# Kernel tuning notes

Hardware: AMD Instinct MI355X
Metric: run time of the kernel (lower is better)

## Reference

```python
import jax, jax.numpy as jnp
import numpy as np

B, S, T, D, H, FF = 2, 512, 64, 256, 8, 1024
DK = D // H
EPS = 1e-5


def setup_inputs() -> dict:
    key = jax.random.key(0)
    ks = jax.random.split(key, 24)
    sc = 1.0 / np.sqrt(D)
    inp = {"x": jax.random.normal(ks[0], (B, S, T, D), jnp.float32)}
    names = ["tq", "tk", "tv", "to", "sq", "sk", "sv", "so"]
    for i, n in enumerate(names):
        inp[n + "_w"] = jax.random.normal(ks[1 + 2 * i], (D, D), jnp.float32) * sc
        inp[n + "_b"] = jax.random.normal(ks[2 + 2 * i], (D,), jnp.float32) * sc
    inp["fc1_w"] = jax.random.normal(ks[17], (D, FF), jnp.float32) * sc
    inp["fc1_b"] = jnp.zeros((FF,), jnp.float32)
    inp["fc2_w"] = jax.random.normal(ks[18], (FF, D), jnp.float32) * (1.0 / np.sqrt(FF))
    inp["fc2_b"] = jnp.zeros((D,), jnp.float32)
    inp["ln1_w"] = jnp.ones((D,), jnp.float32)
    inp["ln1_b"] = jnp.zeros((D,), jnp.float32)
    inp["ln2_w"] = jnp.ones((D,), jnp.float32)
    inp["ln2_b"] = jnp.zeros((D,), jnp.float32)
    return inp


def _heads(x, w, b):
    # (B,S,T,D) -> (B,H,S,T,DK)
    Bx, Sx, Tx, Dx = x.shape
    return (x @ w + b).reshape(Bx, Sx, Tx, H, Dx // H).transpose(0, 3, 1, 2, 4)


def _merge(o, w, b):
    # (B,H,S,T,DK) -> (B,S,T,D)
    Bx, Hx, Sx, Tx, dk = o.shape
    return o.transpose(0, 2, 3, 1, 4).reshape(Bx, Sx, Tx, Hx * dk) @ w + b


def _ln(x, g, b):
    m = jnp.mean(x, -1, keepdims=True)
    v = jnp.mean((x - m) ** 2, -1, keepdims=True)
    return (x - m) * jax.lax.rsqrt(v + EPS) * g + b


def _forward(x, tq_w, tq_b, tk_w, tk_b, tv_w, tv_b, to_w, to_b,
             sq_w, sq_b, sk_w, sk_b, sv_w, sv_b, so_w, so_b,
             fc1_w, fc1_b, fc2_w, fc2_b, ln1_w, ln1_b, ln2_w, ln2_b):
    scale = 1.0 / np.sqrt(DK)
    # --- time attention (over T, independent per space point s) ---
    q = _heads(x, tq_w, tq_b)
    k = _heads(x, tk_w, tk_b)
    v = _heads(x, tv_w, tv_b)
    p = jax.nn.softmax(jnp.einsum('bhstd,bhsud->bhstu', q, k) * scale, axis=-1)
    tt = _merge(jnp.einsum('bhstu,bhsud->bhstd', p, v), to_w, to_b)
    # --- space attention (over S, independent per time step t) ---
    q = _heads(tt, sq_w, sq_b)
    k = _heads(tt, sk_w, sk_b)
    v = _heads(tt, sv_w, sv_b)
    p = jax.nn.softmax(jnp.einsum('bhstd,bhutd->bhtsu', q, k) * scale, axis=-1)
    so = _merge(jnp.einsum('bhtsu,bhutd->bhstd', p, v), so_w, so_b)
    # --- residual + post-LN, then FFN + residual + post-LN ---
    h = _ln(x + so, ln1_w, ln1_b)
    ff = jax.nn.relu(h @ fc1_w + fc1_b) @ fc2_w + fc2_b
    return _ln(h + ff, ln2_w, ln2_b)


def reference(x, tq_w, tq_b, tk_w, tk_b, tv_w, tv_b, to_w, to_b,
              sq_w, sq_b, sk_w, sk_b, sv_w, sv_b, so_w, so_b,
              fc1_w, fc1_b, fc2_w, fc2_b, ln1_w, ln1_b, ln2_w, ln2_b):
    return _forward(x, tq_w, tq_b, tk_w, tk_b, tv_w, tv_b, to_w, to_b,
                    sq_w, sq_b, sk_w, sk_b, sv_w, sv_b, so_w, so_b,
                    fc1_w, fc1_b, fc2_w, fc2_b, ln1_w, ln1_b, ln2_w, ln2_b)
```

## Files before the change

### kernel.cpp

```cpp
#include <hip/hip_runtime.h>
#include <hip/hip_bf16.h>

#define BB   2
#define SS   512
#define TT_  64
#define DD   256
#define HH   8
#define DKK  32
#define FFF  1024
#define NTOK 65536
#define EPSV 1e-5f
#define SCALE 0.17677669529663687f
#define S2F   0.25503486f
#define KPS  40
#define KP   40
#define VH   136
#define VP6  80

typedef unsigned short u16;
typedef unsigned int   u32;
typedef __attribute__((ext_vector_type(8))) short bf16x8;
typedef __attribute__((ext_vector_type(4))) short bf16x4;
typedef __attribute__((ext_vector_type(4))) float f32x4;

#if __has_builtin(__builtin_amdgcn_exp2f)
#define EXP2(x) __builtin_amdgcn_exp2f(x)
#else
#define EXP2(x) exp2f(x)
#endif

__device__ __forceinline__ float bf2f(u32 u) {
    union { u32 i; float f; } c; c.i = u << 16; return c.f;
}
__device__ __forceinline__ u16 f2bf(float f) {
    __hip_bfloat16 h = __float2bfloat16(f);
    return *reinterpret_cast<u16*>(&h);
}
__device__ __forceinline__ u32 cvtpk2(float lo, float hi) {
    float2 f; f.x = lo; f.y = hi;
    __hip_bfloat162 h2 = __float22bfloat162_rn(f);
    union { __hip_bfloat162 h; u32 u; } c; c.h = h2;
    return c.u;
}
__device__ __forceinline__ void load8v(const float* p, float* v) {
    *(float4*)(v)     = *(const float4*)(p);
    *(float4*)(v + 4) = *(const float4*)(p + 4);
}
__device__ __forceinline__ void load8v(const u16* p, float* v) {
    uint4 raw = *(const uint4*)(p);
    v[0] = bf2f(raw.x & 0xffffu); v[1] = bf2f(raw.x >> 16);
    v[2] = bf2f(raw.y & 0xffffu); v[3] = bf2f(raw.y >> 16);
    v[4] = bf2f(raw.z & 0xffffu); v[5] = bf2f(raw.z >> 16);
    v[6] = bf2f(raw.w & 0xffffu); v[7] = bf2f(raw.w >> 16);
}
__device__ __forceinline__ void load4v(const float* p, float* v) {
    float4 t = *(const float4*)p; v[0] = t.x; v[1] = t.y; v[2] = t.z; v[3] = t.w;
}
__device__ __forceinline__ void load4v(const u16* p, float* v) {
    uint2 raw = *(const uint2*)p;
    v[0] = bf2f(raw.x & 0xffffu); v[1] = bf2f(raw.x >> 16);
    v[2] = bf2f(raw.y & 0xffffu); v[3] = bf2f(raw.y >> 16);
}
__device__ __forceinline__ uint4 pack8bf(const float* v) {
    uint4 r;
    r.x = cvtpk2(v[0], v[1]); r.y = cvtpk2(v[2], v[3]);
    r.z = cvtpk2(v[4], v[5]); r.w = cvtpk2(v[6], v[7]);
    return r;
}
__device__ __forceinline__ uint2 pack4bf(const float* v) {
    uint2 r;
    r.x = cvtpk2(v[0], v[1]); r.y = cvtpk2(v[2], v[3]);
    return r;
}
__device__ __forceinline__ bf16x4 packbf4(const float* v) {
    union { uint2 u; bf16x4 h; } c;
    c.u = pack4bf(v);
    return c.h;
}
__device__ __forceinline__ void store4o(float* p, const float* v) {
    float4 t; t.x = v[0]; t.y = v[1]; t.z = v[2]; t.w = v[3];
    *(float4*)p = t;
}
__device__ __forceinline__ void store4o(u16* p, const float* v) {
    *(uint2*)p = pack4bf(v);
}
__device__ __forceinline__ float rload(const float* p) { return *p; }
__device__ __forceinline__ float rload(const u16* p)  { return bf2f(*p); }
__device__ __forceinline__ void sstore(float* p, float v) { *p = v; }
__device__ __forceinline__ void sstore(u16* p, float v)   { *p = f2bf(v); }
__device__ __forceinline__ void gl16(const u16* gsrc, u16* ldst) {
    __builtin_amdgcn_global_load_lds(
        (const __attribute__((address_space(1))) void*)gsrc,
        (__attribute__((address_space(3))) void*)ldst, 16, 0, 0);
}

#if __has_builtin(__builtin_amdgcn_mfma_f32_16x16x16bf16_1k)
__device__ __forceinline__ f32x4 mfma16(bf16x4 a, bf16x4 b, f32x4 c) {
    return __builtin_amdgcn_mfma_f32_16x16x16bf16_1k(a, b, c, 0, 0, 0);
}
#else
__device__ __forceinline__ f32x4 mfma16(bf16x4 a, bf16x4 b, f32x4 c) {
    asm("v_mfma_f32_16x16x16_bf16 %0, %1, %2, %0" : "+v"(c) : "v"(a), "v"(b));
    return c;
}
#endif

#define BF16_ONE ((short)0x3F80)

__global__ __launch_bounds__(256)
void transpose_w(const float* __restrict__ W, u16* __restrict__ WT, int K, int M,
                 float scale)
{
    __shared__ float t[32][33];
    const int mb = blockIdx.x * 32;
    const int kb = blockIdx.y * 32;
    const int lx = threadIdx.x & 31;
    const int ly = threadIdx.x >> 5;
    #pragma unroll
    for (int i = ly; i < 32; i += 8) t[i][lx] = W[(size_t)(kb + i) * M + mb + lx];
    __syncthreads();
    #pragma unroll
    for (int i = ly; i < 32; i += 8) WT[(size_t)(mb + i) * K + kb + lx] = f2bf(t[lx][i] * scale);
}

__global__ __launch_bounds__(256)
void transpose_w4(const float* __restrict__ W0, const float* __restrict__ W1,
                  const float* __restrict__ W2, const float* __restrict__ W3,
                  u16* __restrict__ T0, u16* __restrict__ T1,
                  u16* __restrict__ T2, u16* __restrict__ T3, float s0)
{
    __shared__ float t[32][33];
    const int z = blockIdx.z;
    const float* W = (z == 0) ? W0 : (z == 1) ? W1 : (z == 2) ? W2 : W3;
    u16*       WT = (z == 0) ? T0 : (z == 1) ? T1 : (z == 2) ? T2 : T3;
    const float scale = (z == 0) ? s0 : 1.0f;
    const int mb = blockIdx.x * 32;
    const int kb = blockIdx.y * 32;
    const int lx = threadIdx.x & 31;
    const int ly = threadIdx.x >> 5;
    #pragma unroll
    for (int i = ly; i < 32; i += 8) t[i][lx] = W[(size_t)(kb + i) * DD + mb + lx];
    __syncthreads();
    #pragma unroll
    for (int i = ly; i < 32; i += 8) WT[(size_t)(mb + i) * DD + kb + lx] = f2bf(t[lx][i] * scale);
}

__global__ __launch_bounds__(256)
void pack_bias3(const float* __restrict__ a, const float* __restrict__ b,
                const float* __restrict__ c, float* __restrict__ out, float s0)
{
    const int i = threadIdx.x;
    out[i] = a[i] * s0; out[256 + i] = b[i]; out[512 + i] = c[i];
}

__global__ __launch_bounds__(256)
void fuse_to_sqkv_w(const float* __restrict__ to_w,
                    const float* __restrict__ sq_w, const float* __restrict__ sk_w,
                    const float* __restrict__ sv_w, u16* __restrict__ wt_out)
{
    const int m = blockIdx.x;
    const int k = threadIdx.x;
    const float* Wsq = (m < 256) ? sq_w : (m < 512 ? sk_w : sv_w);
    const int mc = m & 255;
    float acc = 0.f;
    for (int j = 0; j < 256; j++)
        acc += to_w[k * 256 + j] * Wsq[j * 256 + mc];
    if (m < 256) acc *= S2F;
    wt_out[m * 256 + k] = f2bf(acc);
}
__global__ __launch_bounds__(256)
void fuse_to_sqkv_b(const float* __restrict__ to_b,
                    const float* __restrict__ sq_w, const float* __restrict__ sk_w,
                    const float* __restrict__ sv_w,
                    const float* __restrict__ sq_b, const float* __restrict__ sk_b,
                    const float* __restrict__ sv_b, float* __restrict__ b_out)
{
    const int m = blockIdx.x * 256 + threadIdx.x;
    const float* Wsq = (blockIdx.x == 0) ? sq_w : (blockIdx.x == 1 ? sk_w : sv_w);
    const float* bs  = (blockIdx.x == 0) ? sq_b : (blockIdx.x == 1 ? sk_b : sv_b);
    const int mc = m & 255;
    float acc = bs[mc];
    for (int j = 0; j < 256; j++) acc += to_b[j] * Wsq[j * 256 + mc];
    if (blockIdx.x == 0) acc *= S2F;
    b_out[m] = acc;
}

__global__ __launch_bounds__(256)
void cvt_bf16(const float* __restrict__ in, u16* __restrict__ out, int n8)
{
    for (int i = blockIdx.x * blockDim.x + threadIdx.x; i < n8; i += gridDim.x * blockDim.x) {
        float v[8];
        load8v(in + (size_t)i * 8, v);
        *(uint4*)(out + (size_t)i * 8) = pack8bf(v);
    }
}

__global__ __launch_bounds__(512)
void gemm_bt6(const u16* __restrict__ A, int lda,
              const u16* __restrict__ WT,
              const float* __restrict__ bias, u16* __restrict__ C,
              int K, int M, int relu)
{
    __shared__ u16 As0[256 * 32];
    __shared__ u16 As1[256 * 32];
    __shared__ u16 Bs0[128 * 32];
    __shared__ u16 Bs1[128 * 32];
    const int tid  = threadIdx.x;
    const int wid  = tid >> 6;
    const int lane = tid & 63;
    const int l16  = lane & 15;
    const int kg   = lane >> 4;

    const int nwg = gridDim.x * gridDim.y;
    int lin = blockIdx.y * gridDim.x + blockIdx.x;
    lin = (lin & 7) * (nwg >> 3) + (lin >> 3);
    const int row0 = (lin / gridDim.x) * 256;
    const int col0 = (lin % gridDim.x) * 128;

    const int srow = lane >> 2;
    const int gchunk = ((lane & 3) ^ ((srow >> 1) & 3)) * 8;
    const int rchunk = (kg ^ ((l16 >> 1) & 3)) * 8;

    const u16* Abase = A  + (size_t)(row0 + srow) * lda + gchunk;
    const u16* Bbase = WT + (size_t)(col0 + wid * 16 + srow) * K + gchunk;

    f32x4 acc[2][8];
    #pragma unroll
    for (int fr = 0; fr < 2; fr++)
        #pragma unroll
        for (int fc = 0; fc < 8; fc++)
            acc[fr][fc] = (f32x4){0.f, 0.f, 0.f, 0.f};

#define STAGE_T(ASB, BSB, k0)                                                   \
    do {                                                                        \
        _Pragma("unroll")                                                       \
        for (int q = 0; q < 2; q++) {                                           \
            const int rbase = wid * 32 + q * 16;                                \
            gl16(Abase + (size_t)rbase * lda + (k0), &ASB[rbase * 32]);         \
        }                                                                       \
        gl16(Bbase + (k0), &BSB[wid * 16 * 32]);                                \
    } while (0)

#define COMPUTE_T(ASB, BSB)                                                     \
    do {                                                                        \
        bf16x8 af[2], bfr[8];                                                   \
        _Pragma("unroll")                                                       \
        for (int fr = 0; fr < 2; fr++)                                          \
            af[fr] = *(const bf16x8*)(&ASB[(wid * 32 + fr * 16 + l16) * 32 + rchunk]); \
        _Pragma("unroll")                                                       \
        for (int fc = 0; fc < 8; fc++)                                          \
            bfr[fc] = *(const bf16x8*)(&BSB[(fc * 16 + l16) * 32 + rchunk]);    \
        _Pragma("unroll")                                                       \
        for (int fr = 0; fr < 2; fr++)                                          \
            _Pragma("unroll")                                                   \
            for (int fc = 0; fc < 8; fc++)                                      \
                acc[fr][fc] = __builtin_amdgcn_mfma_f32_16x16x32_bf16(af[fr], bfr[fc], acc[fr][fc], 0, 0, 0); \
    } while (0)

    STAGE_T(As0, Bs0, 0);
    __syncthreads();

    for (int k0 = 0; k0 < K; k0 += 64) {
        if (k0 + 32 < K) STAGE_T(As1, Bs1, k0 + 32);
        COMPUTE_T(As0, Bs0);
        __syncthreads();
        if (k0 + 64 < K) STAGE_T(As0, Bs0, k0 + 64);
        COMPUTE_T(As1, Bs1);
        __syncthreads();
    }
#undef STAGE_T
#undef COMPUTE_T

    #pragma unroll
    for (int fr = 0; fr < 2; fr++) {
        #pragma unroll
        for (int fc = 0; fc < 8; fc++) {
            const int col = col0 + fc * 16 + l16;
            const float bv = bias[col];
            const int row = row0 + wid * 32 + fr * 16 + kg * 4;
            #pragma unroll
            for (int j = 0; j < 4; j += 2) {
                float x0 = acc[fr][fc][j]     + bv;
                float x1 = acc[fr][fc][j + 1] + bv;
                if (relu) { x0 = fmaxf(x0, 0.f); x1 = fmaxf(x1, 0.f); }
                const u32 pk = cvtpk2(x0, x1);
                C[(size_t)(row + j)     * M + col] = (u16)pk;
                C[(size_t)(row + j + 1) * M + col] = (u16)(pk >> 16);
            }
        }
    }
}

__global__ __launch_bounds__(512)
void gemm_bt6h(const u16* __restrict__ A, int lda,
               const u16* __restrict__ WT,
               const float* __restrict__ bias, u16* __restrict__ C,
               int K, int M, int relu)
{
    __shared__ u16 As0[128 * 32];
    __shared__ u16 As1[128 * 32];
    __shared__ u16 Bs0[128 * 32];
    __shared__ u16 Bs1[128 * 32];
    const int tid  = threadIdx.x;
    const int wid  = tid >> 6;
    const int lane = tid & 63;
    const int l16  = lane & 15;
    const int kg   = lane >> 4;

    const int nwg = gridDim.x * gridDim.y;
    int lin = blockIdx.y * gridDim.x + blockIdx.x;
    lin = (lin & 7) * (nwg >> 3) + (lin >> 3);
    const int row0 = (lin / gridDim.x) * 128;
    const int col0 = (lin % gridDim.x) * 128;

    const int srow = lane >> 2;
    const int gchunk = ((lane & 3) ^ ((srow >> 1) & 3)) * 8;
    const int rchunk = (kg ^ ((l16 >> 1) & 3)) * 8;

    const u16* Abase = A  + (size_t)(row0 + wid * 16 + srow) * lda + gchunk;
    const u16* Bbase = WT + (size_t)(col0 + wid * 16 + srow) * K + gchunk;

    f32x4 acc[8];
    #pragma unroll
    for (int fc = 0; fc < 8; fc++)
        acc[fc] = (f32x4){0.f, 0.f, 0.f, 0.f};

#define STAGE_H(ASB, BSB, k0)                                                   \
    do {                                                                        \
        gl16(Abase + (k0), &ASB[wid * 16 * 32]);                                \
        gl16(Bbase + (k0), &BSB[wid * 16 * 32]);                                \
    } while (0)

#define COMPUTE_H(ASB, BSB)                                                     \
    do {                                                                        \
        bf16x8 af, bfr[8];                                                      \
        af = *(const bf16x8*)(&ASB[(wid * 16 + l16) * 32 + rchunk]);            \
        _Pragma("unroll")                                                       \
        for (int fc = 0; fc < 8; fc++)                                          \
            bfr[fc] = *(const bf16x8*)(&BSB[(fc * 16 + l16) * 32 + rchunk]);    \
        _Pragma("unroll")                                                       \
        for (int fc = 0; fc < 8; fc++)                                          \
            acc[fc] = __builtin_amdgcn_mfma_f32_16x16x32_bf16(af, bfr[fc], acc[fc], 0, 0, 0); \
    } while (0)

    STAGE_H(As0, Bs0, 0);
    __syncthreads();

    for (int k0 = 0; k0 < K; k0 += 64) {
        if (k0 + 32 < K) STAGE_H(As1, Bs1, k0 + 32);
        COMPUTE_H(As0, Bs0);
        __syncthreads();
        if (k0 + 64 < K) STAGE_H(As0, Bs0, k0 + 64);
        COMPUTE_H(As1, Bs1);
        __syncthreads();
    }
#undef STAGE_H
#undef COMPUTE_H

    #pragma unroll
    for (int fc = 0; fc < 8; fc++) {
        const int col = col0 + fc * 16 + l16;
        const float bv = bias[col];
        const int row = row0 + wid * 16 + kg * 4;
        #pragma unroll
        for (int j = 0; j < 4; j += 2) {
            float x0 = acc[fc][j]     + bv;
            float x1 = acc[fc][j + 1] + bv;
            if (relu) { x0 = fmaxf(x0, 0.f); x1 = fmaxf(x1, 0.f); }
            const u32 pk = cvtpk2(x0, x1);
            C[(size_t)(row + j)     * M + col] = (u16)pk;
            C[(size_t)(row + j + 1) * M + col] = (u16)(pk >> 16);
        }
    }
}

template<typename TR, typename TO>
__global__ __launch_bounds__(512)
void gemm_ln2(const u16* __restrict__ A, int lda,
              const u16* __restrict__ WT,
              const float* __restrict__ bias,
              const TR* __restrict__ R,
              const float* __restrict__ gw, const float* __restrict__ bw,
              TO* __restrict__ out, int K)
{
    __shared__ u16 As0a[256 * 32];
    __shared__ u16 As0b[256 * 32];
    __shared__ u16 As1a[256 * 32];
    __shared__ u16 As1b[256 * 32];
    __shared__ u16 Bs0a[256 * 32];
    __shared__ u16 Bs0b[256 * 32];
    __shared__ u16 Bs1a[256 * 32];
    __shared__ u16 Bs1b[256 * 32];
    const int tid  = threadIdx.x;
    const int wid  = tid >> 6;
    const int lane = tid & 63;
    const int l16  = lane & 15;
    const int kg   = lane >> 4;

    const int nwg = gridDim.x;
    int lin = blockIdx.x;
    lin = (lin & 7) * (nwg >> 3) + (lin >> 3);
    const int row0 = lin * 256;

    const int srow = lane >> 2;
    const int gchunk = ((lane & 3) ^ ((srow >> 1) & 3)) * 8;
    const int rchunk = (kg ^ ((l16 >> 1) & 3)) * 8;

    const u16* Abase = A  + (size_t)(row0 + wid * 32 + srow) * lda + gchunk;
    const u16* Bbase = WT + (size_t)(wid * 32 + srow) * K + gchunk;

    f32x4 acc[2][16];
    #pragma unroll
    for (int fr = 0; fr < 2; fr++)
        #pragma unroll
        for (int fc = 0; fc < 16; fc++)
            acc[fr][fc] = (f32x4){0.f, 0.f, 0.f, 0.f};

#define STAGE_L2(ASA, ASB2, BSA, BSB2, k0)                                      \
    do {                                                                        \
        _Pragma("unroll")                                                       \
        for (int q = 0; q < 2; q++) {                                           \
            const int rbase = wid * 32 + q * 16;                                \
            gl16(Abase + (size_t)(q * 16) * lda + (k0),      &ASA[rbase * 32]); \
            gl16(Abase + (size_t)(q * 16) * lda + (k0) + 32, &ASB2[rbase * 32]);\
            gl16(Bbase + (size_t)(q * 16) * K   + (k0),      &BSA[rbase * 32]); \
            gl16(Bbase + (size_t)(q * 16) * K   + (k0) + 32, &BSB2[rbase * 32]);\
        }                                                                       \
    } while (0)

#define COMPUTE_L2(ASB, BSB)                                                    \
    do {                                                                        \
        bf16x8 af[2];                                                           \
        _Pragma("unroll")                                                       \
        for (int fr = 0; fr < 2; fr++)                                          \
            af[fr] = *(const bf16x8*)(&ASB[(wid * 32 + fr * 16 + l16) * 32 + rchunk]); \
        _Pragma("unroll")                                                       \
        for (int fc = 0; fc < 16; fc++) {                                       \
            bf16x8 bfr = *(const bf16x8*)(&BSB[(fc * 16 + l16) * 32 + rchunk]); \
            acc[0][fc] = __builtin_amdgcn_mfma_f32_16x16x32_bf16(af[0], bfr, acc[0][fc], 0, 0, 0); \
            acc[1][fc] = __builtin_amdgcn_mfma_f32_16x16x32_bf16(af[1], bfr, acc[1][fc], 0, 0, 0); \
        }                                                                       \
    } while (0)

    STAGE_L2(As0a, As0b, Bs0a, Bs0b, 0);
    __syncthreads();

    for (int k0 = 0; k0 < K; k0 += 128) {
        if (k0 + 64 < K) STAGE_L2(As1a, As1b, Bs1a, Bs1b, k0 + 64);
        COMPUTE_L2(As0a, Bs0a);
        COMPUTE_L2(As0b, Bs0b);
        __syncthreads();
        if (k0 + 128 < K) STAGE_L2(As0a, As0b, Bs0a, Bs0b, k0 + 128);
        COMPUTE_L2(As1a, Bs1a);
        COMPUTE_L2(As1b, Bs1b);
        __syncthreads();
    }
#undef STAGE_L2
#undef COMPUTE_L2

    float bia[16], gwv[16], bwv[16];
    #pragma unroll
    for (int fc = 0; fc < 16; fc++) {
        const int d = fc * 16 + l16;
        bia[fc] = bias[d]; gwv[fc] = gw[d]; bwv[fc] = bw[d];
    }
    #pragma unroll
    for (int fr = 0; fr < 2; fr++) {
        #pragma unroll
        for (int j = 0; j < 4; j++) {
            const int row = row0 + wid * 32 + fr * 16 + kg * 4 + j;
            const size_t rb = (size_t)row * DD + l16;
            float v[16];
            float s1 = 0.f, s2 = 0.f;
            #pragma unroll
            for (int fc = 0; fc < 16; fc++) {
                const float xv = acc[fr][fc][j] + bia[fc] + rload(R + rb + fc * 16);
                v[fc] = xv; s1 += xv; s2 += xv * xv;
            }
            #pragma unroll
            for (int o = 1; o < 16; o <<= 1) { s1 += __shfl_xor(s1, o); s2 += __shfl_xor(s2, o); }
            const float mean = s1 * (1.f / DD);
            const float var  = s2 * (1.f / DD) - mean * mean;
            const float rs   = rsqrtf(var + EPSV);
            #pragma unroll
            for (int fc = 0; fc < 16; fc++)
                sstore(out + rb + fc * 16, (v[fc] - mean) * rs * gwv[fc] + bwv[fc]);
        }
    }
}

__global__ __launch_bounds__(256)
void time_attn12(const u16* __restrict__ F, int ld, u16* __restrict__ O)
{
    __shared__ u16 Ks2[2][64 * KP];
    __shared__ u16 Vt2[2][32 * VP6];
    const int bid = blockIdx.x;
    const int tid  = threadIdx.x;
    const int wid  = tid >> 6;
    const int lane = tid & 63;
    const int l16  = lane & 15;
    const int g    = lane >> 4;

    #pragma unroll
    for (int it = 0; it < 2; it++) {
        const int i = tid + it * 256;
        const int tu = i >> 8, rr = (i >> 2) & 63, p = i & 3;
        const int tau = bid * 2 + tu;
        const size_t ga = ((size_t)(tau >> 3) * 64 + rr) * ld + (tau & 7) * DKK + 256 + p * 8;
        *(uint4*)&Ks2[tu][rr * KP + p * 8] = *(const uint4*)(F + ga);
    }
    #pragma unroll
    for (int it = 0; it < 2; it++) {
        const int i = tid + it * 256;
        const int tu = i >> 8, p = (i >> 6) & 3, rr = i & 63;
        const int tau = bid * 2 + tu;
        const size_t ga = ((size_t)(tau >> 3) * 64 + rr) * ld + (tau & 7) * DKK + 512 + p * 8;
        uint4 vv = *(const uint4*)(F + ga);
        const u16* vp = (const u16*)&vv;
        #pragma unroll
        for (int j = 0; j < 8; j++) Vt2[tu][(p * 8 + j) * VP6 + rr] = vp[j];
    }
    __syncthreads();

    const int tu  = wid >> 1;
    const int tau = bid * 2 + tu;
    const int hc  = (tau & 7) * DKK;
    const size_t n0 = (size_t)(tau >> 3) * 64;
    const int q0  = (wid & 1) * 32;
    const f32x4 z4 = (f32x4){0.f, 0.f, 0.f, 0.f};
    const bf16x4 vone = (bf16x4){BF16_ONE, BF16_ONE, BF16_ONE, BF16_ONE};

    bf16x8 qf[2];
    #pragma unroll
    for (int f = 0; f < 2; f++)
        qf[f] = *(const bf16x8*)(F + (n0 + q0 + f * 16 + l16) * ld + hc + g * 8);

    f32x4 s[2][4];
    #pragma unroll
    for (int kt = 0; kt < 4; kt++) {
        bf16x8 kf = *(const bf16x8*)&Ks2[tu][(kt * 16 + l16) * KP + g * 8];
        s[0][kt] = __builtin_amdgcn_mfma_f32_16x16x32_bf16(kf, qf[0], z4, 0, 0, 0);
        s[1][kt] = __builtin_amdgcn_mfma_f32_16x16x32_bf16(kf, qf[1], z4, 0, 0, 0);
    }

    bf16x4 pp[2][4];
    #pragma unroll
    for (int f = 0; f < 2; f++) {
        #pragma unroll
        for (int kt = 0; kt < 4; kt++) {
            float pv[4];
            #pragma unroll
            for (int j = 0; j < 4; j++) pv[j] = EXP2(s[f][kt][j]);
            pp[f][kt] = packbf4(pv);
        }
    }

    f32x4 o[2][2];
    f32x4 lacc[2];
    #pragma unroll
    for (int f = 0; f < 2; f++) {
        lacc[f] = z4;
        #pragma unroll
        for (int hh = 0; hh < 2; hh++)
            o[f][hh] = z4;
    }
    #pragma unroll
    for (int kt = 0; kt < 4; kt++) {
        bf16x4 vf[2];
        #pragma unroll
        for (int hh = 0; hh < 2; hh++)
            vf[hh] = *(const bf16x4*)&Vt2[tu][(hh * 16 + l16) * VP6 + kt * 16 + g * 4];
        #pragma unroll
        for (int f = 0; f < 2; f++) {
            o[f][0] = mfma16(pp[f][kt], vf[0], o[f][0]);
            o[f][1] = mfma16(pp[f][kt], vf[1], o[f][1]);
            lacc[f] = mfma16(pp[f][kt], vone, lacc[f]);
        }
    }

    #pragma unroll
    for (int f = 0; f < 2; f++) {
        float iv[4];
        #pragma unroll
        for (int j = 0; j < 4; j++) iv[j] = 1.f / lacc[f][j];
        #pragma unroll
        for (int hh = 0; hh < 2; hh++) {
            const u32 p0 = cvtpk2(o[f][hh][0] * iv[0], o[f][hh][1] * iv[1]);
            const u32 p1 = cvtpk2(o[f][hh][2] * iv[2], o[f][hh][3] * iv[3]);
            const size_t ga0 = (n0 + q0 + f * 16 + g * 4) * DD + hc + hh * 16 + l16;
            O[ga0]          = (u16)p0;
            O[ga0 + DD]     = (u16)(p0 >> 16);
            O[ga0 + 2 * DD] = (u16)p1;
            O[ga0 + 3 * DD] = (u16)(p1 >> 16);
        }
    }
}

__global__ __launch_bounds__(512, 4)
void space_attn16(u16* __restrict__ F, int ld)
{
    __shared__ u16 Ks[2][128 * KPS];
    __shared__ u16 Vt[2][32 * VH];
    const int bid = blockIdx.x;
    const int t  = bid & (TT_ - 1);
    const int h  = (bid >> 6) & (HH - 1);
    const int b  = bid >> 9;
    const int hc = h * DKK;
    const int tid  = threadIdx.x;
    const int wid  = tid >> 6;
    const int lane = tid & 63;
    const int l16  = lane & 15;
    const int g    = lane >> 4;

    const int kr = tid >> 2, kp = tid & 3;
    const int vr = tid & 127, vp = tid >> 7;
    const size_t rowstr = (size_t)TT_ * ld;
    const size_t base0  = ((size_t)(b * SS) * TT_ + t) * ld + hc;

    const int q0 = wid * 64;
    bf16x8 qf[4];
    #pragma unroll
    for (int f = 0; f < 4; f++) {
        const int s = q0 + f * 16 + l16;
        qf[f] = *(const bf16x8*)(F + base0 + (size_t)s * rowstr + g * 8);
    }

    uint4 kreg = *(const uint4*)(F + base0 + 256 + (size_t)kr * rowstr + kp * 8);
    uint4 vreg = *(const uint4*)(F + base0 + 512 + (size_t)vr * rowstr + vp * 8);
    *(uint4*)&Ks[0][kr * KPS + kp * 8] = kreg;
    {
        const u16* vpp = (const u16*)&vreg;
        #pragma unroll
        for (int j = 0; j < 8; j++) Vt[0][(vp * 8 + j) * VH + vr] = vpp[j];
    }
    __syncthreads();

    f32x4 o[4][2];
    f32x4 lacc[4];
    const f32x4 z4 = (f32x4){0.f, 0.f, 0.f, 0.f};
    const bf16x4 vone = (bf16x4){BF16_ONE, BF16_ONE, BF16_ONE, BF16_ONE};
    #pragma unroll
    for (int f = 0; f < 4; f++) {
        lacc[f] = z4;
        #pragma unroll
        for (int hh = 0; hh < 2; hh++)
            o[f][hh] = z4;
    }

    for (int qtr = 0; qtr < 4; qtr++) {
        const int cur = qtr & 1;
        if (qtr < 3) {
            const int key = (qtr + 1) * 128;
            kreg = *(const uint4*)(F + base0 + 256 + (size_t)(key + kr) * rowstr + kp * 8);
            vreg = *(const uint4*)(F + base0 + 512 + (size_t)(key + vr) * rowstr + vp * 8);
        }

        for (int kc2 = 0; kc2 < 4; kc2++) {
            bf16x8 kfa = *(const bf16x8*)&Ks[cur][(kc2 * 32 +      l16) * KPS + g * 8];
            bf16x8 kfb = *(const bf16x8*)&Ks[cur][(kc2 * 32 + 16 + l16) * KPS + g * 8];

            bf16x4 pa[4], pb[4];
            #pragma unroll
            for (int f = 0; f < 4; f++) {
                f32x4 sa = __builtin_amdgcn_mfma_f32_16x16x32_bf16(kfa, qf[f], z4, 0, 0, 0);
                f32x4 sb = __builtin_amdgcn_mfma_f32_16x16x32_bf16(kfb, qf[f], z4, 0, 0, 0);
                float pva[4], pvb[4];
                #pragma unroll
                for (int j = 0; j < 4; j++) pva[j] = EXP2(sa[j]);
                #pragma unroll
                for (int j = 0; j < 4; j++) pvb[j] = EXP2(sb[j]);
                pa[f] = packbf4(pva);
                pb[f] = packbf4(pvb);
            }

            bf16x4 va[2][2];
            #pragma unroll
            for (int hh = 0; hh < 2; hh++)
                #pragma unroll
                for (int u = 0; u < 2; u++)
                    va[hh][u] = *(const bf16x4*)&Vt[cur][(hh * 16 + l16) * VH + kc2 * 32 + u * 16 + g * 4];

            __builtin_amdgcn_s_setprio(1);
            #pragma unroll
            for (int f = 0; f < 4; f++) {
                #pragma unroll
                for (int hh = 0; hh < 2; hh++) {
                    o[f][hh] = mfma16(pa[f], va[hh][0], o[f][hh]);
                    o[f][hh] = mfma16(pb[f], va[hh][1], o[f][hh]);
                }
                lacc[f] = mfma16(pa[f], vone, lacc[f]);
                lacc[f] = mfma16(pb[f], vone, lacc[f]);
            }
            __builtin_amdgcn_s_setprio(0);
        }

        if (qtr < 3) {
            __syncthreads();
            *(uint4*)&Ks[cur ^ 1][kr * KPS + kp * 8] = kreg;
            const u16* vpp = (const u16*)&vreg;
            #pragma unroll
            for (int j = 0; j < 8; j++) Vt[cur ^ 1][(vp * 8 + j) * VH + vr] = vpp[j];
            __syncthreads();
        }
    }

    #pragma unroll
    for (int f = 0; f < 4; f++) {
        float iv[4];
        #pragma unroll
        for (int j = 0; j < 4; j++) iv[j] = 1.f / lacc[f][j];
        const int s = q0 + f * 16 + g * 4;
        #pragma unroll
        for (int hh = 0; hh < 2; hh++) {
            const u32 p0 = cvtpk2(o[f][hh][0] * iv[0], o[f][hh][1] * iv[1]);
            const u32 p1 = cvtpk2(o[f][hh][2] * iv[2], o[f][hh][3] * iv[3]);
            const size_t ga0 = base0 + (size_t)s * rowstr + hh * 16 + l16;
            F[ga0]              = (u16)p0;
            F[ga0 + rowstr]     = (u16)(p0 >> 16);
            F[ga0 + 2 * rowstr] = (u16)p1;
            F[ga0 + 3 * rowstr] = (u16)(p1 >> 16);
        }
    }
}

template<typename T1, typename TO>
__global__ __launch_bounds__(256)
void add_ln(const T1* __restrict__ X1, const u16* __restrict__ X2,
            const float* __restrict__ gw, const float* __restrict__ bw,
            TO* __restrict__ out)
{
    const int row  = blockIdx.x * 4 + (threadIdx.x >> 6);
    const int lane = threadIdx.x & 63;
    const size_t base = (size_t)row * DD + lane * 4;
    float v[4], w2[4];
    load4v(X1 + base, v);
    load4v(X2 + base, w2);
    v[0] += w2[0]; v[1] += w2[1]; v[2] += w2[2]; v[3] += w2[3];
    float s1 = v[0] + v[1] + v[2] + v[3];
    float s2 = v[0]*v[0] + v[1]*v[1] + v[2]*v[2] + v[3]*v[3];
    #pragma unroll
    for (int o = 1; o < 64; o <<= 1) { s1 += __shfl_xor(s1, o); s2 += __shfl_xor(s2, o); }
    const float mean = s1 * (1.f / DD);
    const float var  = s2 * (1.f / DD) - mean * mean;
    const float rs   = rsqrtf(var + EPSV);
    float o4[4];
    #pragma unroll
    for (int i = 0; i < 4; i++) {
        const int d = lane * 4 + i;
        o4[i] = (v[i] - mean) * rs * gw[d] + bw[d];
    }
    store4o(out + base, o4);
}

extern "C" void kernel_launch(void* const* d_in, const int* in_sizes, int n_in,
                              void* d_out, int out_size, void* d_ws, size_t ws_size,
                              hipStream_t stream)
{
    (void)in_sizes; (void)n_in; (void)out_size;
    const float* x     = (const float*)d_in[0];
    const float* tq_w  = (const float*)d_in[1];
    const float* tq_b  = (const float*)d_in[2];
    const float* tk_w  = (const float*)d_in[3];
    const float* tk_b  = (const float*)d_in[4];
    const float* tv_w  = (const float*)d_in[5];
    const float* tv_b  = (const float*)d_in[6];
    const float* to_w  = (const float*)d_in[7];
    const float* to_b  = (const float*)d_in[8];
    const float* sq_w  = (const float*)d_in[9];
    const float* sq_b  = (const float*)d_in[10];
    const float* sk_w  = (const float*)d_in[11];
    const float* sk_b  = (const float*)d_in[12];
    const float* sv_w  = (const float*)d_in[13];
    const float* sv_b  = (const float*)d_in[14];
    const float* so_w  = (const float*)d_in[15];
    const float* so_b  = (const float*)d_in[16];
    const float* fc1_w = (const float*)d_in[17];
    const float* fc1_b = (const float*)d_in[18];
    const float* fc2_w = (const float*)d_in[19];
    const float* fc2_b = (const float*)d_in[20];
    const float* ln1_w = (const float*)d_in[21];
    const float* ln1_b = (const float*)d_in[22];
    const float* ln2_w = (const float*)d_in[23];
    const float* ln2_b = (const float*)d_in[24];

    const size_t SLOT = (size_t)NTOK * DD;
    u16*   F  = (u16*)d_ws;
    u16*   OA = (u16*)d_out;
    float* HD = (float*)d_out;

    const bool ffn1 = ws_size >= 6 * SLOT * sizeof(u16);
    u16*   WTb = ffn1 ? ((u16*)d_ws + 4 * SLOT)
                      : (u16*)((char*)d_out + (61u << 20));
    float* BIb = ffn1 ? (float*)((u16*)d_ws + 4 * SLOT + 983040)
                      : (float*)((char*)d_out + (63u << 20));

    u16* wt_tqkv  = WTb;
    u16* wt_fused = wt_tqkv + 3 * 65536;
    u16* wt_so    = wt_fused + 3 * 65536;
    u16* wt_fc1   = wt_so + 65536;
    u16* wt_fc2   = wt_fc1 + 262144;
    float* b_tqkv  = BIb;
    float* b_fused = BIb + 768;

    dim3 blk(256);
    dim3 blk5(512);

    transpose_w4<<<dim3(DD / 32, DD / 32, 4), blk, 0, stream>>>(
        tq_w, tk_w, tv_w, so_w,
        wt_tqkv, wt_tqkv + 65536, wt_tqkv + 2 * 65536, wt_so, S2F);
    transpose_w<<<dim3(FFF / 32, DD / 32), blk, 0, stream>>>(fc1_w, wt_fc1, DD, FFF, 1.0f);
    transpose_w<<<dim3(DD / 32, FFF / 32), blk, 0, stream>>>(fc2_w, wt_fc2, FFF, DD, 1.0f);
    pack_bias3<<<1, blk, 0, stream>>>(tq_b, tk_b, tv_b, b_tqkv, S2F);
    fuse_to_sqkv_w<<<768, blk, 0, stream>>>(to_w, sq_w, sk_w, sv_w, wt_fused);
    fuse_to_sqkv_b<<<3, blk, 0, stream>>>(to_b, sq_w, sk_w, sv_w, sq_b, sk_b, sv_b, b_fused);

    cvt_bf16<<<2048, blk, 0, stream>>>(x, OA, (int)(SLOT / 8));

    dim3 gqkv(768 / 128, NTOK / 256);

    gemm_bt6<<<gqkv, blk5, 0, stream>>>(OA, DD, wt_tqkv, b_tqkv, F, DD, 768, 0);
    time_attn12<<<BB * HH * SS / 2, blk, 0, stream>>>(F, 768, OA);

    gemm_bt6<<<gqkv, blk5, 0, stream>>>(OA, DD, wt_fused, b_fused, F, DD, 768, 0);
    space_attn16<<<BB * HH * TT_, blk5, 0, stream>>>(F, 768);

    if (ffn1) {
        u16* HB   = (u16*)d_ws + 5 * SLOT;
        u16* W1FF = (u16*)d_ws;
        gemm_ln2<float, u16><<<NTOK / 256, blk5, 0, stream>>>(
            F, 768, wt_so, so_b, x, ln1_w, ln1_b, HB, DD);
        gemm_bt6<<<dim3(FFF / 128, NTOK / 256), blk5, 0, stream>>>(
            HB, DD, wt_fc1, fc1_b, W1FF, DD, FFF, 1);
        gemm_ln2<u16, float><<<NTOK / 256, blk5, 0, stream>>>(
            W1FF, FFF, wt_fc2, fc2_b, HB, ln2_w, ln2_b, HD, FFF);
    } else {
        u16* W0 = (u16*)d_ws;
        u16* W1 = W0 + SLOT;
        u16* W2 = W1 + SLOT;
        dim3 gd(DD / 128, NTOK / 256);
        gemm_bt6<<<gd, blk5, 0, stream>>>(F, 768, wt_so, so_b, OA, DD, DD, 0);
        add_ln<float, u16><<<NTOK / 4, blk, 0, stream>>>(x, OA, ln1_w, ln1_b, W0);
        for (int c = 0; c < 4; c++) {
            const size_t off = (size_t)c * 16384 * DD;
            gemm_bt6<<<dim3(FFF / 128, 16384 / 256), blk5, 0, stream>>>(W0 + off, DD, wt_fc1, fc1_b, W1, DD, FFF, 1);
            gemm_bt6h<<<dim3(DD / 128, 16384 / 128), blk5, 0, stream>>>(W1, FFF, wt_fc2, fc2_b, W2, FFF, DD, 0);
            add_ln<u16, float><<<16384 / 4, blk, 0, stream>>>(W0 + off, W2, ln2_w, ln2_b, HD + off);
        }
    }
}
```

Measured before the change: 384.9 us.

## Add 256x256-tile GEMM with 64-deep K staging and grouped block remap

Adds a new GEMM kernel that uses 256x256 output tiles (each wave owns 32 rows by 256 columns) instead of 256x128, and stages 64 of K per buffer as two 32-wide halves, double-buffered. Block indices are remapped in strides of eight to change which blocks run together and share cache. The QKV projections and FC1 GEMM are switched to this kernel to raise operand reuse per LDS load and halve the number of K-loop barriers. In exchange it uses 128 KB of LDS and 128 accumulator floats per thread, which lowers occupancy and adds register pressure.

```diff
diff --git a/kernel.cpp b/kernel.cpp
--- a/kernel.cpp
+++ b/kernel.cpp
@@ -192,6 +192,109 @@
         float v[8];
         load8v(in + (size_t)i * 8, v);
         *(uint4*)(out + (size_t)i * 8) = pack8bf(v);
+    }
+}
+
+__global__ __launch_bounds__(512)
+void gemm_bt7(const u16* __restrict__ A, int lda,
+              const u16* __restrict__ WT,
+              const float* __restrict__ bias, u16* __restrict__ C,
+              int K, int M, int relu)
+{
+    __shared__ u16 As0a[256 * 32];
+    __shared__ u16 As0b[256 * 32];
+    __shared__ u16 As1a[256 * 32];
+    __shared__ u16 As1b[256 * 32];
+    __shared__ u16 Bs0a[256 * 32];
+    __shared__ u16 Bs0b[256 * 32];
+    __shared__ u16 Bs1a[256 * 32];
+    __shared__ u16 Bs1b[256 * 32];
+    const int tid  = threadIdx.x;
+    const int wid  = tid >> 6;
+    const int lane = tid & 63;
+    const int l16  = lane & 15;
+    const int kg   = lane >> 4;
+
+    const int gx  = gridDim.x;
+    const int nwg = gridDim.x * gridDim.y;
+    int lin = blockIdx.y * gridDim.x + blockIdx.x;
+    lin = (lin & 7) * (nwg >> 3) + (lin >> 3);
+    const int row0 = (lin / gx) * 256;
+    const int col0 = (lin % gx) * 256;
+
+    const int srow = lane >> 2;
+    const int gchunk = ((lane & 3) ^ ((srow >> 1) & 3)) * 8;
+    const int rchunk = (kg ^ ((l16 >> 1) & 3)) * 8;
+
+    const u16* Abase = A  + (size_t)(row0 + wid * 32 + srow) * lda + gchunk;
+    const u16* Bbase = WT + (size_t)(col0 + wid * 32 + srow) * K + gchunk;
+
+    f32x4 acc[2][16];
+    #pragma unroll
+    for (int fr = 0; fr < 2; fr++)
+        #pragma unroll
+        for (int fc = 0; fc < 16; fc++)
+            acc[fr][fc] = (f32x4){0.f, 0.f, 0.f, 0.f};
+
+#define STAGE_B7(ASA, ASB2, BSA, BSB2, k0)                                      \
+    do {                                                                        \
+        _Pragma("unroll")                                                       \
+        for (int q = 0; q < 2; q++) {                                           \
+            const int rbase = wid * 32 + q * 16;                                \
+            gl16(Abase + (size_t)(q * 16) * lda + (k0),      &ASA[rbase * 32]); \
+            gl16(Abase + (size_t)(q * 16) * lda + (k0) + 32, &ASB2[rbase * 32]);\
+            gl16(Bbase + (size_t)(q * 16) * K   + (k0),      &BSA[rbase * 32]); \
+            gl16(Bbase + (size_t)(q * 16) * K   + (k0) + 32, &BSB2[rbase * 32]);\
+        }                                                                       \
+    } while (0)
+
+#define COMPUTE_B7(ASB, BSB)                                                    \
+    do {                                                                        \
+        bf16x8 af[2];                                                           \
+        _Pragma("unroll")                                                       \
+        for (int fr = 0; fr < 2; fr++)                                          \
+            af[fr] = *(const bf16x8*)(&ASB[(wid * 32 + fr * 16 + l16) * 32 + rchunk]); \
+        _Pragma("unroll")                                                       \
+        for (int fc = 0; fc < 16; fc++) {                                       \
+            bf16x8 bfr = *(const bf16x8*)(&BSB[(fc * 16 + l16) * 32 + rchunk]); \
+            acc[0][fc] = __builtin_amdgcn_mfma_f32_16x16x32_bf16(af[0], bfr, acc[0][fc], 0, 0, 0); \
+            acc[1][fc] = __builtin_amdgcn_mfma_f32_16x16x32_bf16(af[1], bfr, acc[1][fc], 0, 0, 0); \
+        }                                                                       \
+    } while (0)
+
+    STAGE_B7(As0a, As0b, Bs0a, Bs0b, 0);
+    __syncthreads();
+
+    for (int k0 = 0; k0 < K; k0 += 128) {
+        if (k0 + 64 < K) STAGE_B7(As1a, As1b, Bs1a, Bs1b, k0 + 64);
+        COMPUTE_B7(As0a, Bs0a);
+        COMPUTE_B7(As0b, Bs0b);
+        __syncthreads();
+        if (k0 + 128 < K) STAGE_B7(As0a, As0b, Bs0a, Bs0b, k0 + 128);
+        COMPUTE_B7(As1a, Bs1a);
+        COMPUTE_B7(As1b, Bs1b);
+        __syncthreads();
+    }
+#undef STAGE_B7
+#undef COMPUTE_B7
+
+    #pragma unroll
+    for (int fr = 0; fr < 2; fr++) {
+        #pragma unroll
+        for (int fc = 0; fc < 16; fc++) {
+            const int col = col0 + fc * 16 + l16;
+            const float bv = bias[col];
+            const int row = row0 + wid * 32 + fr * 16 + kg * 4;
+            #pragma unroll
+            for (int j = 0; j < 4; j += 2) {
+                float x0 = acc[fr][fc][j]     + bv;
+                float x1 = acc[fr][fc][j + 1] + bv;
+                if (relu) { x0 = fmaxf(x0, 0.f); x1 = fmaxf(x1, 0.f); }
+                const u32 pk = cvtpk2(x0, x1);
+                C[(size_t)(row + j)     * M + col] = (u16)pk;
+                C[(size_t)(row + j + 1) * M + col] = (u16)(pk >> 16);
+            }
+        }
     }
 }
 
@@ -816,12 +919,12 @@
 
     cvt_bf16<<<2048, blk, 0, stream>>>(x, OA, (int)(SLOT / 8));
 
-    dim3 gqkv(768 / 128, NTOK / 256);
-
-    gemm_bt6<<<gqkv, blk5, 0, stream>>>(OA, DD, wt_tqkv, b_tqkv, F, DD, 768, 0);
+    dim3 gqkv7(768 / 256, NTOK / 256);
+
+    gemm_bt7<<<gqkv7, blk5, 0, stream>>>(OA, DD, wt_tqkv, b_tqkv, F, DD, 768, 0);
     time_attn12<<<BB * HH * SS / 2, blk, 0, stream>>>(F, 768, OA);
 
-    gemm_bt6<<<gqkv, blk5, 0, stream>>>(OA, DD, wt_fused, b_fused, F, DD, 768, 0);
+    gemm_bt7<<<gqkv7, blk5, 0, stream>>>(OA, DD, wt_fused, b_fused, F, DD, 768, 0);
     space_attn16<<<BB * HH * TT_, blk5, 0, stream>>>(F, 768);
 
     if (ffn1) {
@@ -829,7 +932,7 @@
         u16* W1FF = (u16*)d_ws;
         gemm_ln2<float, u16><<<NTOK / 256, blk5, 0, stream>>>(
             F, 768, wt_so, so_b, x, ln1_w, ln1_b, HB, DD);
-        gemm_bt6<<<dim3(FFF / 128, NTOK / 256), blk5, 0, stream>>>(
+        gemm_bt7<<<dim3(FFF / 256, NTOK / 256), blk5, 0, stream>>>(
             HB, DD, wt_fc1, fc1_b, W1FF, DD, FFF, 1);
         gemm_ln2<u16, float><<<NTOK / 256, blk5, 0, stream>>>(
             W1FF, FFF, wt_fc2, fc2_b, HB, ln2_w, ln2_b, HD, FFF);
```

Result: no change. 390.1 us (+1.3%).
